# Kernel optimization log

Measured on AMD Instinct MI355X. Metric: run time of the kernel, lower is better.

Reference implementation:

```python
import jax, jax.numpy as jnp
import numpy as np

DIM = 768
NUM_HEADS = 12
HEAD_DIM = DIM // NUM_HEADS
SCALE = HEAD_DIM ** -0.5


def setup_inputs() -> dict:
    key = jax.random.key(0)
    ks = jax.random.split(key, 9)
    B, L, C = 4, 1024, DIM
    x = jax.random.normal(ks[0], (B, L, C), jnp.float32)
    q_ape = jax.random.normal(ks[1], (1, L, C), jnp.float32)
    k_ape = jax.random.normal(ks[2], (1, L, C), jnp.float32)
    attn_pos = jax.random.normal(ks[3], (1, NUM_HEADS, L, L), jnp.float32)
    s = C ** -0.5
    # torch Linear weights: (out_features, in_features)
    Wq = jax.random.normal(ks[4], (C, C), jnp.float32) * s
    Wk = jax.random.normal(ks[5], (C, C), jnp.float32) * s
    Wv = jax.random.normal(ks[6], (C, C), jnp.float32) * s
    Wp = jax.random.normal(ks[7], (C, C), jnp.float32) * s
    bp = jax.random.normal(ks[8], (C,), jnp.float32) * 0.01
    return {"x": x, "q_ape": q_ape, "k_ape": k_ape, "attn_pos": attn_pos,
            "Wq": Wq, "Wk": Wk, "Wv": Wv, "Wp": Wp, "bp": bp}


def _split_heads(t):
    # (B, L, C) -> (B, H, L, D)
    B, L, C = t.shape
    return t.reshape(B, L, NUM_HEADS, HEAD_DIM).transpose(0, 2, 1, 3)


def reference(x, q_ape, k_ape, attn_pos, Wq, Wk, Wv, Wp, bp):
    B, L, C = x.shape
    q = _split_heads((x + q_ape) @ Wq.T)          # (B,H,L,D)
    k = _split_heads((x + k_ape) @ Wk.T)          # (B,H,L,D)
    v = _split_heads(x @ Wv.T)                    # (B,H,L,D)
    attn = jnp.einsum('bhqd,bhkd->bhqk', q, k) * SCALE + attn_pos
    attn = jax.nn.softmax(attn, axis=-1)
    out = jnp.einsum('bhqk,bhkd->bhqd', attn, v)  # (B,H,L,D)
    out = out.transpose(0, 2, 1, 3).reshape(B, L, C)
    return out @ Wp.T + bp
```

## Files before the change

### kernel.cpp

```cpp
#include <hip/hip_runtime.h>
#include <stdint.h>

#define NH 12
#define HD 64
#define NB 4
#define SEQ 1024
#define CDIM 768
#define MTOT (NB*SEQ)
#define MC   (MTOT*CDIM)
#define LC   (SEQ*CDIM)
#define WSZ  (CDIM*CDIM)
#define LST  104
#define EST  136
#define VST  72
#define CST  68
#define L2E  1.44269504f
#define BHSZ (SEQ*HD)

typedef __attribute__((ext_vector_type(4))) float f32x4;
typedef __attribute__((ext_vector_type(8))) __bf16 bf16x8;
typedef __attribute__((ext_vector_type(8))) short short8;
typedef __attribute__((ext_vector_type(4))) unsigned short ushort4v;
typedef unsigned short u16;

static __device__ __forceinline__ f32x4 mfma16(short8 a, short8 b, f32x4 c) {
  return __builtin_amdgcn_mfma_f32_16x16x32_bf16(
      __builtin_bit_cast(bf16x8, a), __builtin_bit_cast(bf16x8, b), c, 0, 0, 0);
}
static __device__ __forceinline__ u16 f2bf(float f) {
  unsigned u = __float_as_uint(f);
  u += 0x7FFFu + ((u >> 16) & 1u);
  return (u16)(u >> 16);
}
static __device__ __forceinline__ float bf2f(u16 h) {
  return __uint_as_float(((unsigned)h) << 16);
}
static __device__ __forceinline__ void lds_load16(const void* g, void* l) {
  __builtin_amdgcn_global_load_lds(
      (const __attribute__((address_space(1))) void*)g,
      (__attribute__((address_space(3))) void*)l, 16, 0, 0);
}

#define PREP_BLKS (MC / 4 / 256)
#define CONV_N4   ((4 * WSZ + CDIM) / 4)
#define CONV_BLKS ((CONV_N4 + 255) / 256)
__global__ __launch_bounds__(256) void prep_all(
    const float* __restrict__ xp, const float* __restrict__ qp,
    const float* __restrict__ kp, const float* __restrict__ Wq,
    const float* __restrict__ Wk, const float* __restrict__ Wv,
    const float* __restrict__ Wp, const float* __restrict__ bp,
    u16* __restrict__ Xq, u16* __restrict__ Xk, u16* __restrict__ Xv,
    u16* __restrict__ Wb) {
  int bid = blockIdx.x;
  if (bid < PREP_BLKS) {
    int i4 = bid * 256 + threadIdx.x;
    int a4 = i4 % (LC / 4);
    f32x4 xx = ((const f32x4*)xp)[i4];
    f32x4 qq = ((const f32x4*)qp)[a4];
    f32x4 kk = ((const f32x4*)kp)[a4];
    ushort4v oq, ok, ov;
#pragma unroll
    for (int j = 0; j < 4; j++) {
      oq[j] = f2bf(xx[j] + qq[j]);
      ok[j] = f2bf(xx[j] + kk[j]);
      ov[j] = f2bf(xx[j]);
    }
    ((ushort4v*)Xq)[i4] = oq;
    ((ushort4v*)Xk)[i4] = ok;
    ((ushort4v*)Xv)[i4] = ov;
  } else {
    int i4 = (bid - PREP_BLKS) * 256 + threadIdx.x;
    if (i4 >= CONV_N4) return;
    int sel = i4 / (WSZ / 4);
    int off = i4 - sel * (WSZ / 4);
    const float* src = sel == 0 ? Wq : sel == 1 ? Wk : sel == 2 ? Wv
                     : sel == 3 ? Wp : bp;
    f32x4 v = ((const f32x4*)src)[off];
    ushort4v o;
#pragma unroll
    for (int j = 0; j < 4; j++) o[j] = f2bf(v[j]);
    ((ushort4v*)Wb)[i4] = o;
  }
}

static __device__ __forceinline__ void gemm_core64(
    const u16* __restrict__ Ab, const u16* __restrict__ Wb,
    short* As, short* Bs, f32x4 acc[2][4]) {
  const int t = threadIdx.x;
  const int lane = t & 63, w = t >> 6, quad = lane >> 4, l16 = lane & 15;
  const int wm = (w >> 1) * 32, wn = (w & 1) * 64;
  const int row4 = t >> 2, chunk = (t & 3) * 8;
  for (int k0 = 0; k0 < CDIM; k0 += 64) {
#pragma unroll
    for (int hh = 0; hh < 2; hh++) {
      const u16* ga = Ab + row4 * CDIM + k0 + hh * 32 + chunk;
      const u16* gb = Wb + row4 * CDIM + k0 + hh * 32 + chunk;
      lds_load16(ga,             (char*)As + hh * 4096 + t * 16);
      lds_load16(gb,             (char*)Bs + hh * 8192 + t * 16);
      lds_load16(gb + 64 * CDIM, (char*)Bs + hh * 8192 + 4096 + t * 16);
    }
    __syncthreads();
#pragma unroll
    for (int hh = 0; hh < 2; hh++) {
      const short* Ah = As + hh * 2048;
      const short* Bh = Bs + hh * 4096;
      short8 af[2], bw[4];
#pragma unroll
      for (int i = 0; i < 2; i++)
        af[i] = *(const short8*)(Ah + (wm + i * 16 + l16) * 32 + quad * 8);
#pragma unroll
      for (int j = 0; j < 4; j++)
        bw[j] = *(const short8*)(Bh + (wn + j * 16 + l16) * 32 + quad * 8);
#pragma unroll
      for (int i = 0; i < 2; i++)
#pragma unroll
        for (int j = 0; j < 4; j++)
          acc[i][j] = mfma16(af[i], bw[j], acc[i][j]);
    }
    __syncthreads();
  }
}

__global__ __launch_bounds__(256) void gemm_qkv(
    const u16* __restrict__ Xq, const u16* __restrict__ Xk, const u16* __restrict__ Xv,
    const u16* __restrict__ Wq, const u16* __restrict__ Wk, const u16* __restrict__ Wv,
    u16* __restrict__ Q, u16* __restrict__ K, u16* __restrict__ Vt) {
  __shared__ __align__(16) short S[12288];
  short* As = S;
  short* Bs = S + 4096;
  const int z = blockIdx.z;
  const int m0 = blockIdx.y * 64, n0 = blockIdx.x * 128;
  const u16* A = (z == 0 ? Xq : z == 1 ? Xk : Xv) + m0 * CDIM;
  const u16* W = (z == 0 ? Wq : z == 1 ? Wk : Wv) + n0 * CDIM;
  f32x4 acc[2][4];
#pragma unroll
  for (int i = 0; i < 2; i++)
#pragma unroll
    for (int j = 0; j < 4; j++) acc[i][j] = 0.f;
  gemm_core64(A, W, As, Bs, acc);

  const int t = threadIdx.x, lane = t & 63, w = t >> 6;
  const int quad = lane >> 4, l16 = lane & 15;
  const int wm = (w >> 1) * 32, wn = (w & 1) * 64;
  const float qs = (z == 0) ? 0.125f : 1.0f;

#pragma unroll
  for (int i = 0; i < 2; i++)
#pragma unroll
    for (int j = 0; j < 4; j++)
#pragma unroll
      for (int r = 0; r < 4; r++) {
        int mr = wm + i * 16 + quad * 4 + r;
        int nc = wn + j * 16 + l16;
        if (z < 2) S[mr * EST + nc] = (short)f2bf(acc[i][j][r] * qs);
        else       S[nc * VST + mr] = (short)f2bf(acc[i][j][r]);
      }
  __syncthreads();

  const int row = t >> 3, ch = t & 7;
  const int b = m0 >> 10, lbase = m0 & 1023;
  if (z == 0) {
#pragma unroll
    for (int cp = 0; cp < 2; cp++) {
      int h = (n0 >> 6) + cp;
#pragma unroll
      for (int rp = 0; rp < 2; rp++) {
        int mr = row + rp * 32;
        short8 v = *(const short8*)(S + mr * EST + cp * 64 + ch * 8);
        *(short8*)(Q + ((((size_t)(b * NH + h)) << 10) + lbase + mr) * HD + ch * 8) = v;
      }
    }
  } else if (z == 1) {
#pragma unroll
    for (int cp = 0; cp < 2; cp++) {
      int h = (n0 >> 6) + cp;
      u16* Kp = K + (size_t)(b * NH + h) * BHSZ;
#pragma unroll
      for (int rp = 0; rp < 2; rp++) {
        int mr = row + rp * 32;
        int tok = lbase + mr;
        short8 v = *(const short8*)(S + mr * EST + cp * 64 + ch * 8);
        *(short8*)(Kp + (((tok >> 4) * 8 + ch) * 16 + (tok & 15)) * 8) = v;
      }
    }
  } else {
#pragma unroll
    for (int rp = 0; rp < 4; rp++) {
      int rn = row + rp * 32;
      int h = (n0 + rn) >> 6, d = rn & 63;
      u16* Vp = Vt + (size_t)(b * NH + h) * BHSZ;
      int jv = d >> 4, ld16 = d & 15;
      int tok = lbase + ch * 8;
      short8 v = *(const short8*)(S + rn * VST + ch * 8);
      *(short8*)(Vp + ((((tok >> 6) * 4 + jv) * 8 + ((tok >> 3) & 7)) * 16 + ld16) * 8) = v;
    }
  }
}

__global__ __launch_bounds__(256, 3) void attn(
    const u16* __restrict__ Q, const u16* __restrict__ Kf, const u16* __restrict__ Vf,
    const float* __restrict__ pos, u16* __restrict__ O) {
  __shared__ __align__(16) short Ps[4 * 16 * LST];
  const int t = threadIdx.x, lane = t & 63, w = t >> 6;
  const int quad = lane >> 4, l16 = lane & 15;
  const int wsub = w & 1, half = w >> 1;

  const int lid = blockIdx.x;
  const int k8 = lid & 7, m = lid >> 3;
  const int g = k8 * 48 + (m >> 2), b = m & 3;
  const int h = g >> 5, qt = g & 31;
  const int bh = b * NH + h;
  const int q0 = qt * 32 + wsub * 16;

  const u16* Kg = Kf + (size_t)bh * BHSZ;
  const u16* Vg = Vf + (size_t)bh * BHSZ;
  const float* Pg = pos + (size_t)(h * SEQ + q0) * SEQ;
  short* Pw = Ps + w * 16 * LST;
  const int fo = quad * 128 + l16 * 8;

  const u16* Qg = Q + ((size_t)bh * SEQ + q0) * HD;
  const short8 qa0 = *(const short8*)(Qg + l16 * HD + quad * 8);
  const short8 qa1 = *(const short8*)(Qg + l16 * HD + 32 + quad * 8);

  f32x4 o[4];
  float lrow[4];
#pragma unroll
  for (int j = 0; j < 4; j++) o[j] = 0.f;
#pragma unroll
  for (int r = 0; r < 4; r++) lrow[r] = 0.f;

  const int kt0 = half * 8;
  short8 kb0[4], kb1[4];
  float pf[16];
#pragma unroll
  for (int j = 0; j < 4; j++) {
    kb0[j] = *(const short8*)(Kg + kt0 * 4096 + j * 1024 + fo);
    kb1[j] = *(const short8*)(Kg + kt0 * 4096 + j * 1024 + 512 + fo);
  }
  {
    const float* pg = Pg + kt0 * 64;
#pragma unroll
    for (int j = 0; j < 4; j++)
#pragma unroll
      for (int r = 0; r < 4; r++)
        pf[j * 4 + r] = pg[(quad * 4 + r) * SEQ + j * 16 + l16] * L2E;
  }

#pragma unroll 1
  for (int kk = 0; kk < 8; ++kk) {
    const int kbase = (kt0 + kk) * 4096;
    short8 vb0[4], vb1[4];
#pragma unroll
    for (int j = 0; j < 4; j++) {
      vb0[j] = *(const short8*)(Vg + kbase + j * 1024 + fo);
      vb1[j] = *(const short8*)(Vg + kbase + j * 1024 + 512 + fo);
    }
    f32x4 s[4];
#pragma unroll
    for (int j = 0; j < 4; j++) {
      f32x4 zz = 0.f;
      s[j] = mfma16(qa1, kb1[j], mfma16(qa0, kb0[j], zz));
    }
#pragma unroll
    for (int j = 0; j < 4; j++)
#pragma unroll
      for (int r = 0; r < 4; r++) {
        float e = __builtin_amdgcn_exp2f(fmaf(s[j][r], L2E, pf[j * 4 + r]));
        unsigned bits = __float_as_uint(e);
        Pw[(quad * 4 + r) * LST + j * 16 + l16] = (short)(bits >> 16);
        lrow[r] += __uint_as_float(bits & 0xFFFF0000u);
      }
    if (kk < 7) {
      const int nb = kbase + 4096;
#pragma unroll
      for (int j = 0; j < 4; j++) {
        kb0[j] = *(const short8*)(Kg + nb + j * 1024 + fo);
        kb1[j] = *(const short8*)(Kg + nb + j * 1024 + 512 + fo);
      }
      const float* pg = Pg + (kt0 + kk + 1) * 64;
#pragma unroll
      for (int j = 0; j < 4; j++)
#pragma unroll
        for (int r = 0; r < 4; r++)
          pf[j * 4 + r] = pg[(quad * 4 + r) * SEQ + j * 16 + l16] * L2E;
    }
    const short8 pa0 = *(const short8*)(Pw + l16 * LST + quad * 8);
    const short8 pa1 = *(const short8*)(Pw + l16 * LST + 32 + quad * 8);
#pragma unroll
    for (int j = 0; j < 4; j++)
      o[j] = mfma16(pa1, vb1[j], mfma16(pa0, vb0[j], o[j]));
  }

#pragma unroll
  for (int off = 1; off < 16; off <<= 1)
#pragma unroll
    for (int r = 0; r < 4; r++) lrow[r] += __shfl_xor(lrow[r], off);

  __syncthreads();
  float* Cb = (float*)Ps;
  const int cb = wsub * (16 * CST + 16);
  if (half) {
#pragma unroll
    for (int j = 0; j < 4; j++)
#pragma unroll
      for (int r = 0; r < 4; r++)
        Cb[cb + (quad * 4 + r) * CST + j * 16 + l16] = o[j][r];
    if (l16 == 0) {
#pragma unroll
      for (int r = 0; r < 4; r++) Cb[cb + 16 * CST + quad * 4 + r] = lrow[r];
    }
  }
  __syncthreads();
  if (half) return;
#pragma unroll
  for (int r = 0; r < 4; r++) lrow[r] += Cb[cb + 16 * CST + quad * 4 + r];
#pragma unroll
  for (int j = 0; j < 4; j++)
#pragma unroll
    for (int r = 0; r < 4; r++)
      o[j][r] += Cb[cb + (quad * 4 + r) * CST + j * 16 + l16];

  u16* Og = O + ((size_t)b * SEQ + q0) * CDIM + h * HD;
  float inv[4];
#pragma unroll
  for (int r = 0; r < 4; r++) inv[r] = 1.0f / lrow[r];
#pragma unroll
  for (int j = 0; j < 4; j++)
#pragma unroll
    for (int r = 0; r < 4; r++)
      Og[(quad * 4 + r) * CDIM + j * 16 + l16] = f2bf(o[j][r] * inv[r]);
}

__global__ __launch_bounds__(256) void gemm_proj(
    const u16* __restrict__ Oin, const u16* __restrict__ Wp,
    const u16* __restrict__ bp, float* __restrict__ out) {
  __shared__ __align__(16) short S[12288];
  const int m0 = blockIdx.y * 64, n0 = blockIdx.x * 128;
  f32x4 acc[2][4];
#pragma unroll
  for (int i = 0; i < 2; i++)
#pragma unroll
    for (int j = 0; j < 4; j++) acc[i][j] = 0.f;
  gemm_core64(Oin + m0 * CDIM, Wp + n0 * CDIM, S, S + 4096, acc);

  const int t = threadIdx.x, lane = t & 63, w = t >> 6;
  const int quad = lane >> 4, l16 = lane & 15;
  const int wm = (w >> 1) * 32, wn = (w & 1) * 64;
#pragma unroll
  for (int i = 0; i < 2; i++) {
    int mrow = m0 + wm + i * 16 + quad * 4;
#pragma unroll
    for (int j = 0; j < 4; j++) {
      int n = n0 + wn + j * 16 + l16;
      float bias = bf2f(bp[n]);
#pragma unroll
      for (int r = 0; r < 4; r++)
        out[(mrow + r) * CDIM + n] = acc[i][j][r] + bias;
    }
  }
}

extern "C" void kernel_launch(void* const* d_in, const int* in_sizes, int n_in,
                              void* d_out, int out_size, void* d_ws, size_t ws_size,
                              hipStream_t stream) {
  (void)in_sizes; (void)n_in; (void)out_size;
  const size_t OFF_XQ = 0, OFF_XK = (size_t)MC, OFF_XV = 2ull * MC,
               OFF_Q = 3ull * MC, OFF_K = 4ull * MC, OFF_VT = 5ull * MC,
               OFF_W = 6ull * MC, TOT = OFF_W + 4ull * WSZ + 1024;
  const size_t NEED = 2 * TOT;
  if (ws_size < NEED) return;

  u16* ws = (u16*)d_ws;
  u16 *Xq = ws + OFF_XQ, *Xk = ws + OFF_XK, *Xv = ws + OFF_XV;
  u16 *Qb = ws + OFF_Q, *Kb = ws + OFF_K, *Vt = ws + OFF_VT;
  u16 *Wb = ws + OFF_W;
  u16 *Wqb = Wb, *Wkb = Wb + WSZ, *Wvb = Wb + 2ull * WSZ,
      *Wpb = Wb + 3ull * WSZ, *bpb = Wb + 4ull * WSZ;
  u16* Ob = Xq;

  prep_all<<<PREP_BLKS + CONV_BLKS, 256, 0, stream>>>(
      (const float*)d_in[0], (const float*)d_in[1], (const float*)d_in[2],
      (const float*)d_in[4], (const float*)d_in[5], (const float*)d_in[6],
      (const float*)d_in[7], (const float*)d_in[8], Xq, Xk, Xv, Wb);
  gemm_qkv<<<dim3(6, 64, 3), 256, 0, stream>>>(Xq, Xk, Xv, Wqb, Wkb, Wvb,
                                               Qb, Kb, Vt);
  attn<<<dim3(1536), 256, 0, stream>>>(Qb, Kb, Vt, (const float*)d_in[3], Ob);
  gemm_proj<<<dim3(6, 64), 256, 0, stream>>>(Ob, Wpb, bpb, (float*)d_out);
}
```

Baseline: 211.8 us.

## Give each attention wave full key range, drop split-K merge, double-buffer bias

The attention kernel changes from splitting the key range across wave pairs (with an LDS merge of partial outputs and row sums) to having each of the four waves handle its own 16 query rows over all 1024 keys. The grid halves to 768 blocks of 64 queries each. The attn_pos bias prefetch becomes two-deep (alternating pfA/pfB), and s_setprio hints are placed around the MFMA blocks. This removes the two block barriers and the cross-wave reduction and doubles K/V reuse per block. In exchange each wave runs a longer serial loop, there are fewer blocks to hide latency, and the extra 16 prefetch registers raise register pressure.

```diff
diff --git a/kernel.cpp b/kernel.cpp
--- a/kernel.cpp
+++ b/kernel.cpp
@@ -13,7 +13,6 @@
 #define LST  104
 #define EST  136
 #define VST  72
-#define CST  68
 #define L2E  1.44269504f
 #define BHSZ (SEQ*HD)
 
@@ -203,14 +202,13 @@
   __shared__ __align__(16) short Ps[4 * 16 * LST];
   const int t = threadIdx.x, lane = t & 63, w = t >> 6;
   const int quad = lane >> 4, l16 = lane & 15;
-  const int wsub = w & 1, half = w >> 1;
 
   const int lid = blockIdx.x;
   const int k8 = lid & 7, m = lid >> 3;
-  const int g = k8 * 48 + (m >> 2), b = m & 3;
-  const int h = g >> 5, qt = g & 31;
+  const int g = k8 * 24 + (m >> 2), b = m & 3;
+  const int h = g >> 4, qt = g & 15;
   const int bh = b * NH + h;
-  const int q0 = qt * 32 + wsub * 16;
+  const int q0 = qt * 64 + w * 16;
 
   const u16* Kg = Kf + (size_t)bh * BHSZ;
   const u16* Vg = Vf + (size_t)bh * BHSZ;
@@ -229,26 +227,23 @@
 #pragma unroll
   for (int r = 0; r < 4; r++) lrow[r] = 0.f;
 
-  const int kt0 = half * 8;
   short8 kb0[4], kb1[4];
-  float pf[16];
+  float pfA[16], pfB[16];
 #pragma unroll
   for (int j = 0; j < 4; j++) {
-    kb0[j] = *(const short8*)(Kg + kt0 * 4096 + j * 1024 + fo);
-    kb1[j] = *(const short8*)(Kg + kt0 * 4096 + j * 1024 + 512 + fo);
-  }
-  {
-    const float* pg = Pg + kt0 * 64;
-#pragma unroll
-    for (int j = 0; j < 4; j++)
-#pragma unroll
-      for (int r = 0; r < 4; r++)
-        pf[j * 4 + r] = pg[(quad * 4 + r) * SEQ + j * 16 + l16] * L2E;
-  }
-
-#pragma unroll 1
-  for (int kk = 0; kk < 8; ++kk) {
-    const int kbase = (kt0 + kk) * 4096;
+    kb0[j] = *(const short8*)(Kg + j * 1024 + fo);
+    kb1[j] = *(const short8*)(Kg + j * 1024 + 512 + fo);
+  }
+#pragma unroll
+  for (int j = 0; j < 4; j++)
+#pragma unroll
+    for (int r = 0; r < 4; r++) {
+      pfA[j * 4 + r] = Pg[(quad * 4 + r) * SEQ + j * 16 + l16] * L2E;
+      pfB[j * 4 + r] = Pg[(quad * 4 + r) * SEQ + 64 + j * 16 + l16] * L2E;
+    }
+
+  auto tile_body = [&](int kt, float (&PF)[16]) {
+    const int kbase = kt * 4096;
     short8 vb0[4], vb1[4];
 #pragma unroll
     for (int j = 0; j < 4; j++) {
@@ -256,69 +251,59 @@
       vb1[j] = *(const short8*)(Vg + kbase + j * 1024 + 512 + fo);
     }
     f32x4 s[4];
+    __builtin_amdgcn_s_setprio(1);
 #pragma unroll
     for (int j = 0; j < 4; j++) {
       f32x4 zz = 0.f;
       s[j] = mfma16(qa1, kb1[j], mfma16(qa0, kb0[j], zz));
     }
+    __builtin_amdgcn_s_setprio(0);
+    {
+      const int nt = kt + 1 < 16 ? kt + 1 : 15;
+      const int nb = nt * 4096;
+#pragma unroll
+      for (int j = 0; j < 4; j++) {
+        kb0[j] = *(const short8*)(Kg + nb + j * 1024 + fo);
+        kb1[j] = *(const short8*)(Kg + nb + j * 1024 + 512 + fo);
+      }
+    }
 #pragma unroll
     for (int j = 0; j < 4; j++)
 #pragma unroll
       for (int r = 0; r < 4; r++) {
-        float e = __builtin_amdgcn_exp2f(fmaf(s[j][r], L2E, pf[j * 4 + r]));
+        float e = __builtin_amdgcn_exp2f(fmaf(s[j][r], L2E, PF[j * 4 + r]));
         unsigned bits = __float_as_uint(e);
         Pw[(quad * 4 + r) * LST + j * 16 + l16] = (short)(bits >> 16);
         lrow[r] += __uint_as_float(bits & 0xFFFF0000u);
       }
-    if (kk < 7) {
-      const int nb = kbase + 4096;
-#pragma unroll
-      for (int j = 0; j < 4; j++) {
-        kb0[j] = *(const short8*)(Kg + nb + j * 1024 + fo);
-        kb1[j] = *(const short8*)(Kg + nb + j * 1024 + 512 + fo);
-      }
-      const float* pg = Pg + (kt0 + kk + 1) * 64;
+    {
+      const int nt = kt + 2 < 16 ? kt + 2 : 15;
+      const float* pg = Pg + nt * 64;
 #pragma unroll
       for (int j = 0; j < 4; j++)
 #pragma unroll
         for (int r = 0; r < 4; r++)
-          pf[j * 4 + r] = pg[(quad * 4 + r) * SEQ + j * 16 + l16] * L2E;
+          PF[j * 4 + r] = pg[(quad * 4 + r) * SEQ + j * 16 + l16] * L2E;
     }
     const short8 pa0 = *(const short8*)(Pw + l16 * LST + quad * 8);
     const short8 pa1 = *(const short8*)(Pw + l16 * LST + 32 + quad * 8);
+    __builtin_amdgcn_s_setprio(1);
 #pragma unroll
     for (int j = 0; j < 4; j++)
       o[j] = mfma16(pa1, vb1[j], mfma16(pa0, vb0[j], o[j]));
+    __builtin_amdgcn_s_setprio(0);
+  };
+
+#pragma unroll 1
+  for (int kp = 0; kp < 8; ++kp) {
+    tile_body(kp * 2,     pfA);
+    tile_body(kp * 2 + 1, pfB);
   }
 
 #pragma unroll
   for (int off = 1; off < 16; off <<= 1)
 #pragma unroll
     for (int r = 0; r < 4; r++) lrow[r] += __shfl_xor(lrow[r], off);
-
-  __syncthreads();
-  float* Cb = (float*)Ps;
-  const int cb = wsub * (16 * CST + 16);
-  if (half) {
-#pragma unroll
-    for (int j = 0; j < 4; j++)
-#pragma unroll
-      for (int r = 0; r < 4; r++)
-        Cb[cb + (quad * 4 + r) * CST + j * 16 + l16] = o[j][r];
-    if (l16 == 0) {
-#pragma unroll
-      for (int r = 0; r < 4; r++) Cb[cb + 16 * CST + quad * 4 + r] = lrow[r];
-    }
-  }
-  __syncthreads();
-  if (half) return;
-#pragma unroll
-  for (int r = 0; r < 4; r++) lrow[r] += Cb[cb + 16 * CST + quad * 4 + r];
-#pragma unroll
-  for (int j = 0; j < 4; j++)
-#pragma unroll
-    for (int r = 0; r < 4; r++)
-      o[j][r] += Cb[cb + (quad * 4 + r) * CST + j * 16 + l16];
 
   u16* Og = O + ((size_t)b * SEQ + q0) * CDIM + h * HD;
   float inv[4];
@@ -384,6 +369,6 @@
       (const float*)d_in[7], (const float*)d_in[8], Xq, Xk, Xv, Wb);
   gemm_qkv<<<dim3(6, 64, 3), 256, 0, stream>>>(Xq, Xk, Xv, Wqb, Wkb, Wvb,
                                                Qb, Kb, Vt);
-  attn<<<dim3(1536), 256, 0, stream>>>(Qb, Kb, Vt, (const float*)d_in[3], Ob);
+  attn<<<dim3(768), 256, 0, stream>>>(Qb, Kb, Vt, (const float*)d_in[3], Ob);
   gemm_proj<<<dim3(6, 64), 256, 0, stream>>>(Ob, Wpb, bpb, (float*)d_out);
 }
```

Result: slower. 264.7 us (+25.0%).
